# Kernel optimization log

Measured on AMD Instinct MI355X. Metric: run time of the kernel, lower is better.

## Reference

```python
import jax, jax.numpy as jnp
import numpy as np

WINDOW = 16  # window_size from init_kwargs


def sigmoid_cutoff(x):
    # max(min(1.2*sigmoid(x) - 0.1, 1), 0)
    return jnp.clip(1.2 * jax.nn.sigmoid(x) - 0.1, 0.0, 1.0)


def setup_inputs() -> dict:
    key = jax.random.key(0)
    k1, k2, k3 = jax.random.split(key, 3)
    B, S, H = 8, 2048, 1024
    x = jax.random.normal(k1, (B, S, H), dtype=jnp.float32)
    # Dense kernels (glorot-ish scale), x_layer has no bias, y_layer has bias
    Wx = jax.random.normal(k2, (H, H), dtype=jnp.float32) * (1.0 / np.sqrt(H))
    Wy = jax.random.normal(k3, (H, 2 * H), dtype=jnp.float32) * (1.0 / np.sqrt(H))
    by = jnp.zeros((2 * H,), dtype=jnp.float32)
    return {"x": x, "Wx": Wx, "Wy": Wy, "by": by}


def reference(x, Wx, Wy, by):
    B, S, H = x.shape
    # left-pad sequence with window_size-1 zeros, then project once (x_layer)
    xp = jnp.pad(x, ((0, 0), (WINDOW - 1, 0), (0, 0)))
    proj = jnp.einsum('bsh,hd->bsd', xp, Wx)  # [B, S+W-1, H]

    def step(state, i):
        # inputs[:, i:S+i] in the original loop
        inp = jax.lax.dynamic_slice_in_dim(proj, i, S, axis=1)  # [B,S,H]
        ns = jnp.einsum('bsh,hd->bsd', state, Wy) + by          # [B,S,2H]
        # reshape [B,S,2,H]: channel 0 = candidate, channel 1 = gate
        cand, gate_logits = jnp.split(ns, 2, axis=-1)
        gate = sigmoid_cutoff(gate_logits)
        new_state = jax.nn.relu(gate * (inp + cand) + (1.0 - gate) * state)
        return new_state, None

    state0 = jnp.zeros_like(x)
    state, _ = jax.lax.scan(step, state0, jnp.arange(WINDOW))
    return state
```

## Files before the change

kernel.cpp:

```cpp
#include <hip/hip_runtime.h>

#define H 1024
#define SEQ 2048
#define MROWS 16384
#define KD 1024
#define LDSW 72

typedef _Float16 f16;
typedef _Float16 f16x8 __attribute__((ext_vector_type(8)));
typedef float f32x4 __attribute__((ext_vector_type(4)));

__device__ __forceinline__ float gate_fn(float x) {
    float s = 1.0f / (1.0f + __expf(-x));
    return fminf(fmaxf(1.2f * s - 0.1f, 0.0f), 1.0f);
}

__device__ __forceinline__ void gload_lds16(const void* g, void* lds) {
    __builtin_amdgcn_global_load_lds(
        (const __attribute__((address_space(1))) unsigned int*)g,
        (__attribute__((address_space(3))) unsigned int*)lds, 16, 0, 0);
}

__global__ void k_f32_to_f16(const float* __restrict__ in, f16* __restrict__ out) {
    size_t i = ((size_t)blockIdx.x * blockDim.x + threadIdx.x) * 8;
    float4 v0 = *(const float4*)(in + i);
    float4 v1 = *(const float4*)(in + i + 4);
    f16x8 o;
    o[0] = (f16)v0.x; o[1] = (f16)v0.y; o[2] = (f16)v0.z; o[3] = (f16)v0.w;
    o[4] = (f16)v1.x; o[5] = (f16)v1.y; o[6] = (f16)v1.z; o[7] = (f16)v1.w;
    *(f16x8*)(out + i) = o;
}

__global__ void k_transpose_f16(const float* __restrict__ Wsrc, f16* __restrict__ WT,
                                int K, int N) {
    __shared__ float tile[32][33];
    int n0 = blockIdx.x * 32, k0 = blockIdx.y * 32;
    for (int i = threadIdx.y; i < 32; i += 8)
        tile[i][threadIdx.x] = Wsrc[(size_t)(k0 + i) * N + n0 + threadIdx.x];
    __syncthreads();
    for (int i = threadIdx.y; i < 32; i += 8)
        WT[(size_t)(n0 + i) * K + k0 + threadIdx.x] = (f16)tile[threadIdx.x][i];
}

__global__ __launch_bounds__(256) void k_proj_gemm(const f16* __restrict__ A,
                                                   const f16* __restrict__ BT,
                                                   f16* __restrict__ P16) {
    __shared__ alignas(16) f16 Alds[128 * 32];
    __shared__ alignas(16) f16 Blds[128 * 32];
    const int tid = threadIdx.x;
    const int lane = tid & 63, wid = tid >> 6;
    const int l15 = lane & 15, l4 = lane >> 4;
    const int bm = blockIdx.x, bn = blockIdx.y;

    const f16* gA[2]; const f16* gB[2];
    char* ldsA[2]; char* ldsB[2];
#pragma unroll
    for (int it = 0; it < 2; ++it) {
        int c = it * 4 + wid;
        int row = c * 16 + (lane >> 2);
        int kch = (lane & 3) ^ ((row >> 1) & 3);
        gA[it] = A + (size_t)(bm * 128 + row) * KD + kch * 8;
        gB[it] = BT + (size_t)(bn * 128 + row) * KD + kch * 8;
        ldsA[it] = (char*)Alds + c * 1024;
        ldsB[it] = (char*)Blds + c * 1024;
    }

    int offA[2], offB[8];
#pragma unroll
    for (int m = 0; m < 2; ++m) {
        int row = wid * 32 + m * 16 + l15;
        offA[m] = row * 64 + ((l4 ^ ((row >> 1) & 3)) << 4);
    }
#pragma unroll
    for (int n = 0; n < 8; ++n) {
        int row = n * 16 + l15;
        offB[n] = row * 64 + ((l4 ^ ((row >> 1) & 3)) << 4);
    }

    f32x4 acc[2][8] = {};

    for (int kt = 0; kt < KD / 32; ++kt) {
        __syncthreads();
#pragma unroll
        for (int it = 0; it < 2; ++it) {
            gload_lds16(gA[it], ldsA[it]);
            gload_lds16(gB[it], ldsB[it]);
            gA[it] += 32; gB[it] += 32;
        }
        __syncthreads();
        f16x8 a[2], b[8];
#pragma unroll
        for (int m = 0; m < 2; ++m) a[m] = *(const f16x8*)((const char*)Alds + offA[m]);
#pragma unroll
        for (int n = 0; n < 8; ++n) b[n] = *(const f16x8*)((const char*)Blds + offB[n]);
#pragma unroll
        for (int n = 0; n < 8; ++n)
#pragma unroll
            for (int m = 0; m < 2; ++m)
                acc[m][n] = __builtin_amdgcn_mfma_f32_16x16x32_f16(a[m], b[n], acc[m][n], 0, 0, 0);
    }

#pragma unroll
    for (int m = 0; m < 2; ++m)
#pragma unroll
        for (int n = 0; n < 8; ++n) {
            int col = bn * 128 + n * 16 + l15;
#pragma unroll
            for (int r = 0; r < 4; ++r) {
                int row = bm * 128 + wid * 32 + m * 16 + l4 * 4 + r;
                P16[(size_t)row * H + col] = (f16)acc[m][n][r];
            }
        }
}

__global__ void k_step0(const f16* __restrict__ P16, const float* __restrict__ by,
                        f16* __restrict__ S16) {
    size_t idx = ((size_t)blockIdx.x * blockDim.x + threadIdx.x) * 8;
    int row = (int)(idx >> 10);
    int d = (int)(idx & 1023);
    int s = row & (SEQ - 1);
    f16x8 p = {};
    if (s >= 15) p = *(const f16x8*)(P16 + (size_t)(row - 15) * H + d);
    float4 byc0 = *(const float4*)(by + d);
    float4 byc1 = *(const float4*)(by + d + 4);
    float4 byg0 = *(const float4*)(by + H + d);
    float4 byg1 = *(const float4*)(by + H + d + 4);
    f16x8 sv;
#pragma unroll
    for (int j = 0; j < 8; ++j) {
        float byc = (j < 4) ? ((const float*)&byc0)[j] : ((const float*)&byc1)[j - 4];
        float byg = (j < 4) ? ((const float*)&byg0)[j] : ((const float*)&byg1)[j - 4];
        float g = gate_fn(byg);
        float v = fmaxf(g * ((float)p[j] + byc), 0.f);
        sv[j] = (f16)v;
    }
    *(f16x8*)(S16 + idx) = sv;
}

__global__ __launch_bounds__(256) void k_step_gemm(const f16* __restrict__ A,
                                                   const f16* __restrict__ BT,
                                                   const f16* __restrict__ P16,
                                                   const float* __restrict__ by,
                                                   float* __restrict__ Out,
                                                   f16* __restrict__ Snext,
                                                   int stepi) {
    __shared__ alignas(16) char ldsraw[2 * 128 * LDSW * 2];
    f16* Alds = (f16*)ldsraw;
    f16* Blds = (f16*)(ldsraw + 8192);
    f16* Cand = (f16*)ldsraw;
    f16* Gate = (f16*)(ldsraw + 128 * LDSW * 2);

    const int tid = threadIdx.x;
    const int lane = tid & 63, wid = tid >> 6;
    const int l15 = lane & 15, l4 = lane >> 4;

    const int nwg = gridDim.x;
    const int orig = blockIdx.x;
    const int wg = (orig & 7) * (nwg >> 3) + (orig >> 3);
    const int t = wg & 15;
    const int bm = wg >> 4;

    const f16* gA[2]; const f16* gB[2];
    char* ldsA[2]; char* ldsB[2];
#pragma unroll
    for (int it = 0; it < 2; ++it) {
        int c = it * 4 + wid;
        int row = c * 16 + (lane >> 2);
        int kch = (lane & 3) ^ ((row >> 1) & 3);
        gA[it] = A + (size_t)(bm * 128 + row) * KD + kch * 8;
        int rowB = t * 64 + row + (row >= 64 ? 960 : 0);
        gB[it] = BT + (size_t)rowB * KD + kch * 8;
        ldsA[it] = (char*)Alds + c * 1024;
        ldsB[it] = (char*)Blds + c * 1024;
    }

    int offA[2], offB[8];
#pragma unroll
    for (int m = 0; m < 2; ++m) {
        int row = wid * 32 + m * 16 + l15;
        offA[m] = row * 64 + ((l4 ^ ((row >> 1) & 3)) << 4);
    }
#pragma unroll
    for (int n = 0; n < 8; ++n) {
        int row = n * 16 + l15;
        offB[n] = row * 64 + ((l4 ^ ((row >> 1) & 3)) << 4);
    }

    f32x4 acc[2][8] = {};

    for (int kt = 0; kt < KD / 32; ++kt) {
        __syncthreads();
#pragma unroll
        for (int it = 0; it < 2; ++it) {
            gload_lds16(gA[it], ldsA[it]);
            gload_lds16(gB[it], ldsB[it]);
            gA[it] += 32; gB[it] += 32;
        }
        __syncthreads();
        f16x8 a[2], b[8];
#pragma unroll
        for (int m = 0; m < 2; ++m) a[m] = *(const f16x8*)((const char*)Alds + offA[m]);
#pragma unroll
        for (int n = 0; n < 8; ++n) b[n] = *(const f16x8*)((const char*)Blds + offB[n]);
#pragma unroll
        for (int n = 0; n < 8; ++n)
#pragma unroll
            for (int m = 0; m < 2; ++m)
                acc[m][n] = __builtin_amdgcn_mfma_f32_16x16x32_f16(a[m], b[n], acc[m][n], 0, 0, 0);
    }

    __syncthreads();
#pragma unroll
    for (int m = 0; m < 2; ++m)
#pragma unroll
        for (int n = 0; n < 4; ++n)
#pragma unroll
            for (int r = 0; r < 4; ++r) {
                int row = wid * 32 + m * 16 + l4 * 4 + r;
                int col = n * 16 + l15;
                Cand[row * LDSW + col] = (f16)acc[m][n][r];
                Gate[row * LDSW + col] = (f16)acc[m][n + 4][r];
            }
    __syncthreads();

    const bool last = (stepi == 15);
    const int rl0 = tid >> 3;
    const int dl = (tid & 7) * 8;
    const int dg = t * 64 + dl;
    float4 byc0 = *(const float4*)(by + dg);
    float4 byc1 = *(const float4*)(by + dg + 4);
    float4 byg0 = *(const float4*)(by + H + dg);
    float4 byg1 = *(const float4*)(by + H + dg + 4);
#pragma unroll
    for (int p = 0; p < 4; ++p) {
        int rl = p * 32 + rl0;
        int grow = bm * 128 + rl;
        int s = grow & (SEQ - 1);
        f16x8 c8 = *(const f16x8*)(Cand + rl * LDSW + dl);
        f16x8 g8 = *(const f16x8*)(Gate + rl * LDSW + dl);
        f16x8 p8 = {};
        if (s >= 15 - stepi)
            p8 = *(const f16x8*)(P16 + (size_t)(grow + stepi - 15) * H + dg);
        f16x8 s8 = *(const f16x8*)(A + (size_t)grow * H + dg);
        f16x8 o8;
        float ov[8];
#pragma unroll
        for (int j = 0; j < 8; ++j) {
            float byc = (j < 4) ? ((const float*)&byc0)[j] : ((const float*)&byc1)[j - 4];
            float byg = (j < 4) ? ((const float*)&byg0)[j] : ((const float*)&byg1)[j - 4];
            float cand = (float)c8[j] + byc;
            float g = gate_fn((float)g8[j] + byg);
            float v = fmaxf(g * ((float)p8[j] + cand) + (1.f - g) * (float)s8[j], 0.f);
            o8[j] = (f16)v;
            ov[j] = v;
        }
        *(f16x8*)(Snext + (size_t)grow * H + dg) = o8;
        if (last) {
            float4 w0 = make_float4(ov[0], ov[1], ov[2], ov[3]);
            float4 w1 = make_float4(ov[4], ov[5], ov[6], ov[7]);
            *(float4*)(Out + (size_t)grow * H + dg) = w0;
            *(float4*)(Out + (size_t)grow * H + dg + 4) = w1;
        }
    }
}

extern "C" void kernel_launch(void* const* d_in, const int* in_sizes, int n_in,
                              void* d_out, int out_size, void* d_ws, size_t ws_size,
                              hipStream_t stream) {
    (void)in_sizes; (void)n_in; (void)out_size; (void)ws_size;
    const float* x  = (const float*)d_in[0];
    const float* Wx = (const float*)d_in[1];
    const float* Wy = (const float*)d_in[2];
    const float* by = (const float*)d_in[3];
    float* out = (float*)d_out;

    char* ws = (char*)d_ws;
    const size_t MB = 1024ull * 1024ull;
    f16* st16a = (f16*)(ws);
    f16* st16b = (f16*)(ws + 32 * MB);
    f16* P16   = (f16*)(ws + 64 * MB);
    f16* WxT   = (f16*)(ws + 96 * MB);
    f16* WyT   = (f16*)(ws + 98 * MB);

    hipLaunchKernelGGL(k_f32_to_f16, dim3(MROWS * H / 8 / 256), dim3(256), 0, stream, x, st16a);
    hipLaunchKernelGGL(k_transpose_f16, dim3(H / 32, H / 32), dim3(32, 8), 0, stream, Wx, WxT, H, H);
    hipLaunchKernelGGL(k_transpose_f16, dim3(2 * H / 32, H / 32), dim3(32, 8), 0, stream, Wy, WyT, H, 2 * H);
    hipLaunchKernelGGL(k_proj_gemm, dim3(MROWS / 128, H / 128), dim3(256), 0, stream, st16a, WxT, P16);
    hipLaunchKernelGGL(k_step0, dim3(MROWS * H / 8 / 256), dim3(256), 0, stream, P16, by, st16b);
    f16* bufs[2] = {st16a, st16b};
    for (int i = 1; i <= 15; ++i) {
        const f16* cur = bufs[i & 1];
        f16* nxt = bufs[(i + 1) & 1];
        hipLaunchKernelGGL(k_step_gemm, dim3(MROWS / 128 * 16), dim3(256), 0, stream,
                           cur, WyT, P16, by, out, nxt, i);
    }
}
```

Baseline: 1.467 ms.

## Enlarge step GEMM tiles to 256x256 with triple-buffered LDS pipeline

Replaces the 128x128-tile, 256-thread step GEMM with a 256-row by 256-column (128 candidate plus 128 gate) tile using 512 threads and 8 waves. The K loop now keeps three LDS buffers and prefetches two tiles ahead with direct global-to-LDS loads and explicit vmcnt waits, so global loads overlap the MFMA work. The epilogue runs in two rounds through LDS, and the last step skips the f16 state write. Bigger tiles raise arithmetic intensity and cut redundant global traffic. The cost is 96KB of LDS and a large accumulator array, which limits occupancy to about one block per CU.

```diff
diff --git a/kernel.cpp b/kernel.cpp
--- a/kernel.cpp
+++ b/kernel.cpp
@@ -4,6 +4,9 @@
 #define SEQ 2048
 #define MROWS 16384
 #define KD 1024
+#define BK 32
+#define NT (KD / BK)
+#define EPW 72
 #define LDSW 72
 
 typedef _Float16 f16;
@@ -137,131 +140,135 @@
     *(f16x8*)(S16 + idx) = sv;
 }
 
-__global__ __launch_bounds__(256) void k_step_gemm(const f16* __restrict__ A,
-                                                   const f16* __restrict__ BT,
-                                                   const f16* __restrict__ P16,
-                                                   const float* __restrict__ by,
-                                                   float* __restrict__ Out,
-                                                   f16* __restrict__ Snext,
-                                                   int stepi) {
-    __shared__ alignas(16) char ldsraw[2 * 128 * LDSW * 2];
-    f16* Alds = (f16*)ldsraw;
-    f16* Blds = (f16*)(ldsraw + 8192);
-    f16* Cand = (f16*)ldsraw;
-    f16* Gate = (f16*)(ldsraw + 128 * LDSW * 2);
-
+__global__ __launch_bounds__(512) void k_step_gemm256(const f16* __restrict__ A,
+                                                      const f16* __restrict__ BT,
+                                                      const f16* __restrict__ P16,
+                                                      const float* __restrict__ by,
+                                                      float* __restrict__ Out,
+                                                      f16* __restrict__ Snext,
+                                                      int stepi) {
+    __shared__ alignas(16) char lds[98304];
     const int tid = threadIdx.x;
-    const int lane = tid & 63, wid = tid >> 6;
+    const int lane = tid & 63, w = tid >> 6;
     const int l15 = lane & 15, l4 = lane >> 4;
-
-    const int nwg = gridDim.x;
+    const int wr = w >> 2, wc = w & 3;
+
     const int orig = blockIdx.x;
-    const int wg = (orig & 7) * (nwg >> 3) + (orig >> 3);
-    const int t = wg & 15;
-    const int bm = wg >> 4;
-
-    const f16* gA[2]; const f16* gB[2];
-    char* ldsA[2]; char* ldsB[2];
-#pragma unroll
-    for (int it = 0; it < 2; ++it) {
-        int c = it * 4 + wid;
-        int row = c * 16 + (lane >> 2);
-        int kch = (lane & 3) ^ ((row >> 1) & 3);
-        gA[it] = A + (size_t)(bm * 128 + row) * KD + kch * 8;
-        int rowB = t * 64 + row + (row >= 64 ? 960 : 0);
-        gB[it] = BT + (size_t)rowB * KD + kch * 8;
-        ldsA[it] = (char*)Alds + c * 1024;
-        ldsB[it] = (char*)Blds + c * 1024;
-    }
-
-    int offA[2], offB[8];
-#pragma unroll
-    for (int m = 0; m < 2; ++m) {
-        int row = wid * 32 + m * 16 + l15;
-        offA[m] = row * 64 + ((l4 ^ ((row >> 1) & 3)) << 4);
-    }
-#pragma unroll
-    for (int n = 0; n < 8; ++n) {
-        int row = n * 16 + l15;
-        offB[n] = row * 64 + ((l4 ^ ((row >> 1) & 3)) << 4);
-    }
-
-    f32x4 acc[2][8] = {};
-
-    for (int kt = 0; kt < KD / 32; ++kt) {
-        __syncthreads();
-#pragma unroll
-        for (int it = 0; it < 2; ++it) {
-            gload_lds16(gA[it], ldsA[it]);
-            gload_lds16(gB[it], ldsB[it]);
-            gA[it] += 32; gB[it] += 32;
+    const int wg = (orig & 7) * 64 + (orig >> 3);
+    const int bm = wg >> 3, nb = wg & 7;
+
+    const int rA0 = w * 16 + (lane >> 2);
+    const int rA1 = rA0 + 128;
+    const char* pA0 = (const char*)A + ((size_t)(bm * 256 + rA0) * KD + (((lane & 3) ^ ((rA0 >> 1) & 3)) * 8)) * 2;
+    const char* pA1 = (const char*)A + ((size_t)(bm * 256 + rA1) * KD + (((lane & 3) ^ ((rA1 >> 1) & 3)) * 8)) * 2;
+    const int gB0 = ((rA0 >> 5) & 1) * H + nb * 128 + (rA0 >> 6) * 32 + (rA0 & 31);
+    const int gB1 = ((rA1 >> 5) & 1) * H + nb * 128 + (rA1 >> 6) * 32 + (rA1 & 31);
+    const char* pB0 = (const char*)BT + ((size_t)gB0 * KD + (((lane & 3) ^ ((rA0 >> 1) & 3)) * 8)) * 2;
+    const char* pB1 = (const char*)BT + ((size_t)gB1 * KD + (((lane & 3) ^ ((rA1 >> 1) & 3)) * 8)) * 2;
+
+    const int dstoff = w * 1024 + lane * 16;
+    char* cb = lds;
+    char* nbuf = lds + 32768;
+    char* sb = lds + 65536;
+
+#define STAGE_TILE(lb) do {                                  \
+        gload_lds16(pA0, (lb) + dstoff);                     \
+        gload_lds16(pA1, (lb) + 8192 + dstoff);              \
+        gload_lds16(pB0, (lb) + 16384 + dstoff);             \
+        gload_lds16(pB1, (lb) + 24576 + dstoff);             \
+        pA0 += 64; pA1 += 64; pB0 += 64; pB1 += 64; } while (0)
+
+    const int sx = (l4 ^ ((l15 >> 1) & 3)) << 4;
+    int offA[8], offB[4];
+#pragma unroll
+    for (int m = 0; m < 8; ++m) offA[m] = (wr * 128 + m * 16 + l15) * 64 + sx;
+#pragma unroll
+    for (int n = 0; n < 4; ++n) offB[n] = (wc * 64 + n * 16 + l15) * 64 + sx;
+
+    f32x4 acc[8][4] = {};
+
+    STAGE_TILE(cb);
+    STAGE_TILE(nbuf);
+    asm volatile("s_waitcnt vmcnt(4)" ::: "memory");
+    __builtin_amdgcn_sched_barrier(0);
+    __syncthreads();
+
+    for (int t = 0; t < NT; ++t) {
+        if (t + 2 < NT) STAGE_TILE(sb);
+        f16x8 a[8], b[4];
+#pragma unroll
+        for (int m = 0; m < 8; ++m) a[m] = *(const f16x8*)(cb + offA[m]);
+#pragma unroll
+        for (int n = 0; n < 4; ++n) b[n] = *(const f16x8*)(cb + 16384 + offB[n]);
+        __builtin_amdgcn_s_setprio(1);
+#pragma unroll
+        for (int m = 0; m < 8; ++m)
+#pragma unroll
+            for (int n = 0; n < 4; ++n)
+                acc[m][n] = __builtin_amdgcn_mfma_f32_16x16x32_f16(a[m], b[n], acc[m][n], 0, 0, 0);
+        __builtin_amdgcn_s_setprio(0);
+        if (t + 2 < NT) { asm volatile("s_waitcnt vmcnt(4)" ::: "memory"); }
+        else           { asm volatile("s_waitcnt vmcnt(0)" ::: "memory"); }
+        __builtin_amdgcn_sched_barrier(0);
+        __syncthreads();
+        char* tmp = cb; cb = nbuf; nbuf = sb; sb = tmp;
+    }
+
+    const bool last = (stepi == 15);
+    f16* Cand = (f16*)lds;
+    f16* Gate = (f16*)(lds + 256 * EPW * 2);
+#pragma unroll
+    for (int rnd = 0; rnd < 2; ++rnd) {
+#pragma unroll
+        for (int m = 0; m < 8; ++m)
+#pragma unroll
+            for (int r4 = 0; r4 < 4; ++r4) {
+                int row = wr * 128 + m * 16 + l4 * 4 + r4;
+                int cr = wc * 16 + l15;
+                Cand[row * EPW + cr] = (f16)acc[m][rnd][r4];
+                Gate[row * EPW + cr] = (f16)acc[m][rnd + 2][r4];
+            }
+        __syncthreads();
+        const int g = tid & 7;
+        const int rb = tid >> 3;
+        const int ctile = (g >> 1) * 32 + rnd * 16 + (g & 1) * 8;
+        const int d = nb * 128 + ctile;
+        const int cr0 = g * 8;
+        float4 byc0 = *(const float4*)(by + d);
+        float4 byc1 = *(const float4*)(by + d + 4);
+        float4 byg0 = *(const float4*)(by + H + d);
+        float4 byg1 = *(const float4*)(by + H + d + 4);
+#pragma unroll
+        for (int p = 0; p < 4; ++p) {
+            int row = p * 64 + rb;
+            int grow = bm * 256 + row;
+            int s = grow & (SEQ - 1);
+            f16x8 c8 = *(const f16x8*)(Cand + row * EPW + cr0);
+            f16x8 g8 = *(const f16x8*)(Gate + row * EPW + cr0);
+            f16x8 p8 = {};
+            if (s >= 15 - stepi)
+                p8 = *(const f16x8*)(P16 + (size_t)(grow + stepi - 15) * H + d);
+            f16x8 s8 = *(const f16x8*)(A + (size_t)grow * H + d);
+            f16x8 o8; float ov[8];
+#pragma unroll
+            for (int j = 0; j < 8; ++j) {
+                float byc = (j < 4) ? ((const float*)&byc0)[j] : ((const float*)&byc1)[j - 4];
+                float byg = (j < 4) ? ((const float*)&byg0)[j] : ((const float*)&byg1)[j - 4];
+                float cand = (float)c8[j] + byc;
+                float gg = gate_fn((float)g8[j] + byg);
+                float v = fmaxf(gg * ((float)p8[j] + cand) + (1.f - gg) * (float)s8[j], 0.f);
+                o8[j] = (f16)v; ov[j] = v;
+            }
+            if (!last) {
+                *(f16x8*)(Snext + (size_t)grow * H + d) = o8;
+            } else {
+                *(float4*)(Out + (size_t)grow * H + d) = make_float4(ov[0], ov[1], ov[2], ov[3]);
+                *(float4*)(Out + (size_t)grow * H + d + 4) = make_float4(ov[4], ov[5], ov[6], ov[7]);
+            }
         }
         __syncthreads();
-        f16x8 a[2], b[8];
-#pragma unroll
-        for (int m = 0; m < 2; ++m) a[m] = *(const f16x8*)((const char*)Alds + offA[m]);
-#pragma unroll
-        for (int n = 0; n < 8; ++n) b[n] = *(const f16x8*)((const char*)Blds + offB[n]);
-#pragma unroll
-        for (int n = 0; n < 8; ++n)
-#pragma unroll
-            for (int m = 0; m < 2; ++m)
-                acc[m][n] = __builtin_amdgcn_mfma_f32_16x16x32_f16(a[m], b[n], acc[m][n], 0, 0, 0);
-    }
-
-    __syncthreads();
-#pragma unroll
-    for (int m = 0; m < 2; ++m)
-#pragma unroll
-        for (int n = 0; n < 4; ++n)
-#pragma unroll
-            for (int r = 0; r < 4; ++r) {
-                int row = wid * 32 + m * 16 + l4 * 4 + r;
-                int col = n * 16 + l15;
-                Cand[row * LDSW + col] = (f16)acc[m][n][r];
-                Gate[row * LDSW + col] = (f16)acc[m][n + 4][r];
-            }
-    __syncthreads();
-
-    const bool last = (stepi == 15);
-    const int rl0 = tid >> 3;
-    const int dl = (tid & 7) * 8;
-    const int dg = t * 64 + dl;
-    float4 byc0 = *(const float4*)(by + dg);
-    float4 byc1 = *(const float4*)(by + dg + 4);
-    float4 byg0 = *(const float4*)(by + H + dg);
-    float4 byg1 = *(const float4*)(by + H + dg + 4);
-#pragma unroll
-    for (int p = 0; p < 4; ++p) {
-        int rl = p * 32 + rl0;
-        int grow = bm * 128 + rl;
-        int s = grow & (SEQ - 1);
-        f16x8 c8 = *(const f16x8*)(Cand + rl * LDSW + dl);
-        f16x8 g8 = *(const f16x8*)(Gate + rl * LDSW + dl);
-        f16x8 p8 = {};
-        if (s >= 15 - stepi)
-            p8 = *(const f16x8*)(P16 + (size_t)(grow + stepi - 15) * H + dg);
-        f16x8 s8 = *(const f16x8*)(A + (size_t)grow * H + dg);
-        f16x8 o8;
-        float ov[8];
-#pragma unroll
-        for (int j = 0; j < 8; ++j) {
-            float byc = (j < 4) ? ((const float*)&byc0)[j] : ((const float*)&byc1)[j - 4];
-            float byg = (j < 4) ? ((const float*)&byg0)[j] : ((const float*)&byg1)[j - 4];
-            float cand = (float)c8[j] + byc;
-            float g = gate_fn((float)g8[j] + byg);
-            float v = fmaxf(g * ((float)p8[j] + cand) + (1.f - g) * (float)s8[j], 0.f);
-            o8[j] = (f16)v;
-            ov[j] = v;
-        }
-        *(f16x8*)(Snext + (size_t)grow * H + dg) = o8;
-        if (last) {
-            float4 w0 = make_float4(ov[0], ov[1], ov[2], ov[3]);
-            float4 w1 = make_float4(ov[4], ov[5], ov[6], ov[7]);
-            *(float4*)(Out + (size_t)grow * H + dg) = w0;
-            *(float4*)(Out + (size_t)grow * H + dg + 4) = w1;
-        }
-    }
+    }
+#undef STAGE_TILE
 }
 
 extern "C" void kernel_launch(void* const* d_in, const int* in_sizes, int n_in,
@@ -287,11 +294,12 @@
     hipLaunchKernelGGL(k_transpose_f16, dim3(2 * H / 32, H / 32), dim3(32, 8), 0, stream, Wy, WyT, H, 2 * H);
     hipLaunchKernelGGL(k_proj_gemm, dim3(MROWS / 128, H / 128), dim3(256), 0, stream, st16a, WxT, P16);
     hipLaunchKernelGGL(k_step0, dim3(MROWS * H / 8 / 256), dim3(256), 0, stream, P16, by, st16b);
+
     f16* bufs[2] = {st16a, st16b};
     for (int i = 1; i <= 15; ++i) {
         const f16* cur = bufs[i & 1];
         f16* nxt = bufs[(i + 1) & 1];
-        hipLaunchKernelGGL(k_step_gemm, dim3(MROWS / 128 * 16), dim3(256), 0, stream,
+        hipLaunchKernelGGL(k_step_gemm256, dim3(MROWS / 256 * 8), dim3(512), 0, stream,
                            cur, WyT, P16, by, out, nxt, i);
     }
 }
```

Result: faster. 1.387 ms (-5.5%).
